# Kernel optimization log

Hardware: AMD Instinct MI355X
Metric: run time of the kernel (lower is better)

## Reference

```python
import jax, jax.numpy as jnp
import numpy as np

B, T, C = 32, 512, 1024
H, D = 16, 64
BLOCK_SIZE = 512


def setup_inputs() -> dict:
    key = jax.random.key(0)
    ks = jax.random.split(key, 6)
    s_in = 1.0 / np.sqrt(C)
    return {
        "x": jax.random.normal(ks[0], (B, T, C), dtype=jnp.float32),
        "wq": jax.random.normal(ks[1], (H, C, D), dtype=jnp.float32) * s_in,
        "wk": jax.random.normal(ks[2], (H, C, D), dtype=jnp.float32) * s_in,
        "wv": jax.random.normal(ks[3], (H, C, D), dtype=jnp.float32) * s_in,
        "w_proj": jax.random.normal(ks[4], (C, C), dtype=jnp.float32) * s_in,
        "b_proj": jax.random.normal(ks[5], (C,), dtype=jnp.float32) * 0.01,
    }


def reference(x, wq, wk, wv, w_proj, b_proj):
    b, t, c = x.shape
    # per-head projections (bias=False Linears stacked on head axis)
    q = jnp.einsum("btc,hcd->bhtd", x, wq)
    k = jnp.einsum("btc,hcd->bhtd", x, wk)
    v = jnp.einsum("btc,hcd->bhtd", x, wv)
    # NOTE: original scales by 1/sqrt(C) with C = n_embd, not head_size
    scale = 1.0 / (c ** 0.5)
    scores = jnp.einsum("bhtd,bhsd->bhts", q, k) * scale  # [B,H,T,T]
    causal = jnp.tril(jnp.ones((t, t), dtype=bool))
    scores = jnp.where(causal, scores, jnp.finfo(scores.dtype).min)
    attn = jax.nn.softmax(scores, axis=-1)
    out = jnp.einsum("bhts,bhsd->bhtd", attn, v)
    # concat heads in order -> [B,T,H*D]
    out = out.transpose(0, 2, 1, 3).reshape(b, t, -1)
    # output projection (dropout = identity in eval mode)
    return out @ w_proj + b_proj
```

## Files before the change

kernel.cpp:

```cpp
#include <hip/hip_runtime.h>

typedef unsigned int u32;
typedef unsigned short u16;
typedef __bf16 bf16x8 __attribute__((ext_vector_type(8)));
typedef float f32x4 __attribute__((ext_vector_type(4)));
typedef u16 u16x8 __attribute__((ext_vector_type(8)));
typedef u16 u16x4 __attribute__((ext_vector_type(4)));

#define DEVI static __device__ __forceinline__

DEVI u16 f2bf(float f) {
  union { float f; u32 u; } v; v.f = f;
  return (u16)((v.u + 0x7fffu + ((v.u >> 16) & 1u)) >> 16);
}

DEVI u32 cvtpk(float a, float b) {
  u32 r;
  asm("v_cvt_pk_bf16_f32 %0, %1, %2" : "=v"(r) : "v"(a), "v"(b));
  return r;
}

constexpr long QS_ = 16777216;
constexpr long XB_O    = 0;
constexpr long WQKV_O  = 16777216;
constexpr long Q_O     = 19922944;
constexpr long CTX_O   = 70254592;
constexpr long WPROJ_O = 87031808;

#define SCL_Q 0.045084220027780106f

__global__ __launch_bounds__(256) void k_prep_all(const float* __restrict__ x,
                                                  const float* __restrict__ wq,
                                                  const float* __restrict__ wk,
                                                  const float* __restrict__ wv,
                                                  const float* __restrict__ wp,
                                                  u16* __restrict__ ws) {
  __shared__ float tile[64][65];
  const int b = blockIdx.x;
  const int tid = threadIdx.x;
  if (b < 1024) {
    const float* src;
    u16* dst;
    long srs;
    if (b < 768) {
      int sel = b >> 8, rest = b & 255, h = rest >> 4, kt = rest & 15;
      const float* W = (sel == 0) ? wq : ((sel == 1) ? wk : wv);
      src = W + (long)(h * 1024 + kt * 64) * 64;
      srs = 64;
      dst = ws + WQKV_O + (long)(sel * 1024 + h * 64) * 1024 + kt * 64;
    } else {
      int b3 = b - 768, ntile = b3 >> 4, kt = b3 & 15;
      src = wp + (long)(kt * 64) * 1024 + ntile * 64;
      srs = 1024;
      dst = ws + WPROJ_O + (long)(ntile * 64) * 1024 + kt * 64;
    }
    #pragma unroll
    for (int i = 0; i < 4; ++i) {
      int idx = i * 256 + tid, r = idx >> 4, c4 = idx & 15;
      float4 v = *(const float4*)(src + (long)r * srs + c4 * 4);
      tile[r][c4 * 4 + 0] = v.x; tile[r][c4 * 4 + 1] = v.y;
      tile[r][c4 * 4 + 2] = v.z; tile[r][c4 * 4 + 3] = v.w;
    }
    __syncthreads();
    #pragma unroll
    for (int i = 0; i < 2; ++i) {
      int idx = i * 256 + tid, dr = idx >> 3, c8 = idx & 7;
      u16x8 o8;
      #pragma unroll
      for (int j = 0; j < 8; ++j) o8[j] = f2bf(tile[c8 * 8 + j][dr]);
      *(u16x8*)(dst + (long)dr * 1024 + c8 * 8) = o8;
    }
  } else {
    long id = (long)(b - 1024) * 256 + tid;
    const float4* p = (const float4*)(x + id * 8);
    float4 a = p[0], c = p[1];
    u16x8 r;
    r[0]=f2bf(a.x); r[1]=f2bf(a.y); r[2]=f2bf(a.z); r[3]=f2bf(a.w);
    r[4]=f2bf(c.x); r[5]=f2bf(c.y); r[6]=f2bf(c.z); r[7]=f2bf(c.w);
    *(u16x8*)(ws + XB_O + id * 8) = r;
  }
}

DEVI void gload16(const u16* g, u16* l) {
  __builtin_amdgcn_global_load_lds((const __attribute__((address_space(1))) u32*)g,
                                   (__attribute__((address_space(3))) u32*)l, 16, 0, 0);
}

template <int NN, int EPI, int PANELS>
__global__ __launch_bounds__(512, 2)
void k_gemm(const u16* __restrict__ A, const u16* __restrict__ Bt,
            u16* __restrict__ oq, float* __restrict__ of, const float* __restrict__ bias) {
  __shared__ u16 lds[2][4][8192];

  const int tid = threadIdx.x;
  const int lane = tid & 63;
  const int w = tid >> 6;
  const int wm = w >> 2, wn = w & 3;
  const int lg = lane >> 4, lr = lane & 15;
  const int bht = 2 + (wn >> 1);
  const int bn0 = (wn & 1) * 4;

  constexpr int NBG = NN / 256 / PANELS;
  constexpr int NG = 16 * PANELS;
  const int nwg = gridDim.x;
  const int swz = ((int)blockIdx.x & 7) * (nwg >> 3) + ((int)blockIdx.x >> 3);
  const int bm = swz / NBG, bng = swz % NBG;
  const long m0 = (long)bm * 256;

  int srcoff[2];
  #pragma unroll
  for (int r2 = 0; r2 < 2; ++r2) {
    int s = r2 * 8 + w;
    int mi = s >> 1, ks = s & 1;
    int rowl = mi * 16 + (lane >> 2);
    int colu = ks * 32 + (((lane & 3) * 8) ^ (((lane >> 5) & 1) * 16));
    srcoff[r2] = rowl * 1024 + colu;
  }
  const int fo = lr * 32 + ((lg * 8) ^ (((lr >> 3) & 1) * 16));

  const u16* At    = A  + m0 * 1024;
  const u16* Bbase = Bt + (long)bng * PANELS * 262144;

  f32x4 acc[8][4] = {};
  bf16x8 aq[2][2][2];
  bf16x8 bfr[4][2];

#define STAGE(buf_, ht_, gbase_)                                               \
  { _Pragma("unroll") for (int r_ = 0; r_ < 2; ++r_)                           \
      gload16((gbase_) + srcoff[r_], &lds[buf_][ht_][r_ * 4096 + w * 512]); }

#define LDS_AQ(set_, buf_, q_)                                                 \
  { _Pragma("unroll") for (int i_ = 0; i_ < 2; ++i_)                           \
    _Pragma("unroll") for (int ks_ = 0; ks_ < 2; ++ks_)                        \
      aq[set_][i_][ks_] = *(const bf16x8*)&lds[buf_][wm][(((q_)*2 + i_) * 2 + ks_) * 512 + fo]; }

#define LDS_BF(buf_, lo_)                                                      \
  { _Pragma("unroll") for (int j_ = 0; j_ < 2; ++j_)                           \
    _Pragma("unroll") for (int ks_ = 0; ks_ < 2; ++ks_)                        \
      bfr[(lo_) + j_][ks_] = *(const bf16x8*)&lds[buf_][bht][((bn0 + (lo_) + j_) * 2 + ks_) * 512 + fo]; }

#define QUAD8(set_, q_, lo_)                                                   \
  { __builtin_amdgcn_s_setprio(1);                                             \
    _Pragma("unroll") for (int ks_ = 0; ks_ < 2; ++ks_)                        \
    _Pragma("unroll") for (int i_ = 0; i_ < 2; ++i_)                           \
    _Pragma("unroll") for (int j_ = 0; j_ < 2; ++j_)                           \
      acc[(q_)*2 + i_][(lo_) + j_] = __builtin_amdgcn_mfma_f32_16x16x32_bf16(  \
          aq[set_][i_][ks_], bfr[(lo_) + j_][ks_], acc[(q_)*2 + i_][(lo_) + j_], 0, 0, 0); \
    __builtin_amdgcn_s_setprio(0); }

#define BARF() { asm volatile("s_barrier" ::: "memory"); }

  auto epilogue = [&](int p) {
    const int n0 = (bng * PANELS + p) * 256;
    if constexpr (EPI == 0) {
      #pragma unroll
      for (int mi = 0; mi < 8; ++mi) {
        int grow = (int)m0 + wm * 128 + mi * 16 + lg * 4;
        int b = grow >> 9, t0 = grow & 511;
        #pragma unroll
        for (int ni = 0; ni < 4; ++ni) {
          int gcol = n0 + wn * 64 + ni * 16 + lr;
          int sel = gcol >> 10, h = (gcol >> 6) & 15, d = gcol & 63;
          float scl = (sel == 0) ? SCL_Q : 1.0f;
          u16* dst = oq + (long)sel * QS_ + (((long)(b * 16 + h) * 512 + t0) * 64 + d);
          #pragma unroll
          for (int r = 0; r < 4; ++r) dst[r * 64] = f2bf(acc[mi][ni][r] * scl);
        }
      }
    } else {
      float bv[4];
      #pragma unroll
      for (int ni = 0; ni < 4; ++ni) bv[ni] = bias[n0 + wn * 64 + ni * 16 + lr];
      #pragma unroll
      for (int mi = 0; mi < 8; ++mi) {
        int grow = (int)m0 + wm * 128 + mi * 16 + lg * 4;
        #pragma unroll
        for (int ni = 0; ni < 4; ++ni) {
          int gcol = n0 + wn * 64 + ni * 16 + lr;
          #pragma unroll
          for (int r = 0; r < 4; ++r)
            of[(long)(grow + r) * NN + gcol] = acc[mi][ni][r] + bv[ni];
        }
      }
    }
  };

  STAGE(0, 0, At);
  STAGE(0, 1, At + 131072);
  STAGE(0, 2, Bbase);
  STAGE(0, 3, Bbase + 131072);
  STAGE(1, 0, At + 64);
  STAGE(1, 1, At + 131072 + 64);
  STAGE(1, 2, Bbase + 64);
  STAGE(1, 3, Bbase + 131072 + 64);
  asm volatile("s_waitcnt vmcnt(8)" ::: "memory");
  BARF();
  LDS_AQ(0, 0, 0);
  LDS_BF(0, 0);

  #pragma unroll 1
  for (int g = 0; g < NG; ++g) {
    const int buf = g & 1;
    const u16* Asrc = At + ((g + 2) & 15) * 64;
    const u16* Bsrc = Bbase + (long)((g + 2) >> 4) * 262144 + ((g + 2) & 15) * 64;

    LDS_BF(buf, 2);
    LDS_AQ(1, buf, 1);
    QUAD8(0, 0, 0);
    BARF();
    QUAD8(0, 0, 2);
    BARF();
    LDS_AQ(0, buf, 2);
    if (g + 2 < NG) { STAGE(buf, 2, Bsrc); STAGE(buf, 3, Bsrc + 131072); }
    QUAD8(1, 1, 0);
    BARF();
    QUAD8(1, 1, 2);
    BARF();
    LDS_AQ(1, buf, 3);
    QUAD8(0, 2, 0);
    BARF();
    QUAD8(0, 2, 2);
    asm volatile("s_waitcnt lgkmcnt(0)" ::: "memory");
    __builtin_amdgcn_sched_barrier(0);
    BARF();
    if (g + 2 < NG) { STAGE(buf, 0, Asrc); STAGE(buf, 1, Asrc + 131072); }
    QUAD8(1, 3, 0);
    BARF();
    if (g < NG - 2)       { asm volatile("s_waitcnt vmcnt(8)" ::: "memory"); }
    else if (g == NG - 2) { asm volatile("s_waitcnt vmcnt(0)" ::: "memory"); }
    BARF();
    if (g + 1 < NG) {
      LDS_AQ(0, buf ^ 1, 0);
      LDS_BF(buf ^ 1, 0);
    }
    QUAD8(1, 3, 2);
    BARF();

    if ((g & 15) == 15) {
      epilogue(g >> 4);
      if (g + 1 < NG) {
        #pragma unroll
        for (int mi = 0; mi < 8; ++mi)
          #pragma unroll
          for (int ni = 0; ni < 4; ++ni) acc[mi][ni] = f32x4{0.f, 0.f, 0.f, 0.f};
      }
    }
  }
#undef STAGE
#undef LDS_AQ
#undef LDS_BF
#undef QUAD8
#undef BARF
}

__global__ __launch_bounds__(256, 3)
void k_attn(const u16* __restrict__ Qp, const u16* __restrict__ Kp,
            const u16* __restrict__ Vp, u16* __restrict__ ctx) {
  __shared__ u16 k_lds[2][64 * 72];
  __shared__ u16 vt_lds[2][64 * 72];

  const int bid = blockIdx.x;
  const int qi = 3 - (bid >> 9);
  const int bh = bid & 511;
  const int tid = threadIdx.x, lane = tid & 63, w = tid >> 6;
  const int lg = lane >> 4, lr = lane & 15;
  const long base = (long)bh * (512 * 64);

  const int q0 = qi * 128 + w * 32;

#define LBAR() { asm volatile("s_waitcnt lgkmcnt(0)" ::: "memory");            \
                 __builtin_amdgcn_sched_barrier(0);                            \
                 asm volatile("s_barrier" ::: "memory"); }

  bf16x8 qf[2][2];
  #pragma unroll
  for (int mt = 0; mt < 2; ++mt)
    #pragma unroll
    for (int k2 = 0; k2 < 2; ++k2)
      qf[mt][k2] = *(const bf16x8*)(Qp + base + (long)(q0 + mt * 16 + lr) * 64 + k2 * 32 + lg * 8);

  f32x4 o[2][4] = {};
  float ls[2] = {0.f, 0.f};
  u32 pkw[2][4][2];

  const int nch = (qi + 1) * 2;
  int srow[2], scol[2], cslot[2];
  #pragma unroll
  for (int i = 0; i < 2; ++i) {
    int s = i * 256 + tid;
    srow[i] = s >> 3; scol[i] = s & 7;
    int sr = srow[i];
    cslot[i] = ((sr >> 5) << 5) + (((sr >> 2) & 3) << 3) + (((sr >> 4) & 1) << 2) + (sr & 3);
  }

  uint4 kreg[2], vreg[2];
  auto loadch = [&](int c) {
    #pragma unroll
    for (int i = 0; i < 2; ++i) {
      long go = base + (long)(c * 64 + srow[i]) * 64 + scol[i] * 8;
      kreg[i] = *(const uint4*)(Kp + go);
      vreg[i] = *(const uint4*)(Vp + go);
    }
  };
  auto writech = [&](int bsel) {
    #pragma unroll
    for (int i = 0; i < 2; ++i) {
      *(uint4*)&k_lds[bsel][srow[i] * 72 + scol[i] * 8] = kreg[i];
      union { uint4 v; u16 s[8]; } t; t.v = vreg[i];
      #pragma unroll
      for (int j = 0; j < 8; ++j)
        vt_lds[bsel][(scol[i] * 8 + j) * 72 + cslot[i]] = t.s[j];
    }
  };
  auto pv_step = [&](int vsel) {
    bf16x8 vf2[4][2];
    #pragma unroll
    for (int dt = 0; dt < 4; ++dt)
      #pragma unroll
      for (int k2 = 0; k2 < 2; ++k2)
        vf2[dt][k2] = *(const bf16x8*)&vt_lds[vsel][(dt * 16 + lr) * 72 + k2 * 32 + lg * 8];
    __builtin_amdgcn_s_setprio(1);
    #pragma unroll
    for (int k2 = 0; k2 < 2; ++k2)
      #pragma unroll
      for (int mt = 0; mt < 2; ++mt) {
        union { u32 w4[4]; bf16x8 v; } pb;
        pb.w4[0] = pkw[mt][2 * k2][0];
        pb.w4[1] = pkw[mt][2 * k2][1];
        pb.w4[2] = pkw[mt][2 * k2 + 1][0];
        pb.w4[3] = pkw[mt][2 * k2 + 1][1];
        #pragma unroll
        for (int dt = 0; dt < 4; ++dt)
          o[mt][dt] = __builtin_amdgcn_mfma_f32_16x16x32_bf16(vf2[dt][k2], pb.v, o[mt][dt], 0, 0, 0);
      }
    __builtin_amdgcn_s_setprio(0);
  };

  loadch(0);
  writech(0);
  loadch(1);
  __syncthreads();

  #pragma unroll 1
  for (int c = 0; c < nch; ++c) {
    const int bsel = c & 1;
    const bool doQK = (c * 64 <= q0 + 31);
    const bool doPV = (c >= 1) && ((c - 1) * 64 <= q0 + 31);

    bf16x8 kf2[4][2];
    if (doQK) {
      #pragma unroll
      for (int nt = 0; nt < 4; ++nt)
        #pragma unroll
        for (int k2 = 0; k2 < 2; ++k2)
          kf2[nt][k2] = *(const bf16x8*)&k_lds[bsel][(nt * 16 + lr) * 72 + k2 * 32 + lg * 8];
    }

    if (doPV) pv_step(bsel ^ 1);

    f32x4 st[2][4] = {};
    if (doQK) {
      __builtin_amdgcn_s_setprio(1);
      #pragma unroll
      for (int k2 = 0; k2 < 2; ++k2)
        #pragma unroll
        for (int mt = 0; mt < 2; ++mt)
          #pragma unroll
          for (int nt = 0; nt < 4; ++nt)
            st[mt][nt] = __builtin_amdgcn_mfma_f32_16x16x32_bf16(kf2[nt][k2], qf[mt][k2], st[mt][nt], 0, 0, 0);
      __builtin_amdgcn_s_setprio(0);

      const bool full = (c * 64 + 63 <= q0);
      #pragma unroll
      for (int mt = 0; mt < 2; ++mt) {
        const int q = q0 + mt * 16 + lr;
        if (!full) {
          #pragma unroll
          for (int nt = 0; nt < 4; ++nt)
            #pragma unroll
            for (int r = 0; r < 4; ++r) {
              int s_ = c * 64 + nt * 16 + lg * 4 + r;
              st[mt][nt][r] = (s_ <= q) ? st[mt][nt][r] : -1e30f;
            }
        }
        float ps = 0.f;
        float p[4][4];
        #pragma unroll
        for (int nt = 0; nt < 4; ++nt)
          #pragma unroll
          for (int r = 0; r < 4; ++r) {
            float pv = exp2f(st[mt][nt][r]);
            p[nt][r] = pv;
            ps += pv;
          }
        ls[mt] += ps;
        #pragma unroll
        for (int nt = 0; nt < 4; ++nt) {
          pkw[mt][nt][0] = cvtpk(p[nt][0], p[nt][1]);
          pkw[mt][nt][1] = cvtpk(p[nt][2], p[nt][3]);
        }
      }
    }

    LBAR();
    if (c + 1 < nch) writech(bsel ^ 1);
    if (c + 2 < nch) loadch(c + 2);
    LBAR();
  }

  if ((nch - 1) * 64 <= q0 + 31) pv_step((nch - 1) & 1);

  const int b = bh >> 4, h = bh & 15;
  #pragma unroll
  for (int mt = 0; mt < 2; ++mt) {
    float l = ls[mt];
    l += __shfl_xor(l, 16);
    l += __shfl_xor(l, 32);
    const float inv = 1.0f / l;
    const int t = q0 + mt * 16 + lr;
    #pragma unroll
    for (int dt = 0; dt < 4; ++dt) {
      u16x4 pk4;
      #pragma unroll
      for (int r = 0; r < 4; ++r) pk4[r] = f2bf(o[mt][dt][r] * inv);
      *(u16x4*)(ctx + ((long)(b * 512 + t)) * 1024 + h * 64 + dt * 16 + lg * 4) = pk4;
    }
  }
#undef LBAR
}

extern "C" void kernel_launch(void* const* d_in, const int* in_sizes, int n_in,
                              void* d_out, int out_size, void* d_ws, size_t ws_size,
                              hipStream_t stream) {
  const float* x  = (const float*)d_in[0];
  const float* wq = (const float*)d_in[1];
  const float* wk = (const float*)d_in[2];
  const float* wv = (const float*)d_in[3];
  const float* wp = (const float*)d_in[4];
  const float* bp = (const float*)d_in[5];
  float* out = (float*)d_out;
  u16* ws = (u16*)d_ws;

  u16* XB    = ws + XB_O;
  u16* WQKV  = ws + WQKV_O;
  u16* Qb    = ws + Q_O;
  u16* CTX   = ws + CTX_O;
  u16* WPROJ = ws + WPROJ_O;

  k_prep_all<<<9216, 256, 0, stream>>>(x, wq, wk, wv, wp, ws);
  k_gemm<3072, 0, 3><<<256, 512, 0, stream>>>(XB, WQKV, Qb, nullptr, nullptr);
  k_attn<<<2048, 256, 0, stream>>>(Qb, Qb + QS_, Qb + 2 * QS_, CTX);
  k_gemm<1024, 1, 1><<<256, 512, 0, stream>>>(CTX, WPROJ, nullptr, out, bp);
}
```

Baseline: 220.5 us.

## Double attention block to 256 query rows with 8 waves sharing K/V tiles

Measured after the change: 232.2 us. +5.3%, slower.

```diff
diff --git a/kernel.cpp b/kernel.cpp
--- a/kernel.cpp
+++ b/kernel.cpp
@@ -253,20 +253,20 @@
 #undef BARF
 }
 
-__global__ __launch_bounds__(256, 3)
+__global__ __launch_bounds__(512, 2)
 void k_attn(const u16* __restrict__ Qp, const u16* __restrict__ Kp,
             const u16* __restrict__ Vp, u16* __restrict__ ctx) {
   __shared__ u16 k_lds[2][64 * 72];
   __shared__ u16 vt_lds[2][64 * 72];
 
   const int bid = blockIdx.x;
-  const int qi = 3 - (bid >> 9);
+  const int half = 1 - (bid >> 9);
   const int bh = bid & 511;
   const int tid = threadIdx.x, lane = tid & 63, w = tid >> 6;
   const int lg = lane >> 4, lr = lane & 15;
   const long base = (long)bh * (512 * 64);
 
-  const int q0 = qi * 128 + w * 32;
+  const int q0 = half * 256 + w * 32;
 
 #define LBAR() { asm volatile("s_waitcnt lgkmcnt(0)" ::: "memory");            \
                  __builtin_amdgcn_sched_barrier(0);                            \
@@ -283,34 +283,22 @@
   float ls[2] = {0.f, 0.f};
   u32 pkw[2][4][2];
 
-  const int nch = (qi + 1) * 2;
-  int srow[2], scol[2], cslot[2];
-  #pragma unroll
-  for (int i = 0; i < 2; ++i) {
-    int s = i * 256 + tid;
-    srow[i] = s >> 3; scol[i] = s & 7;
-    int sr = srow[i];
-    cslot[i] = ((sr >> 5) << 5) + (((sr >> 2) & 3) << 3) + (((sr >> 4) & 1) << 2) + (sr & 3);
-  }
-
-  uint4 kreg[2], vreg[2];
+  const int nch = (half + 1) * 4;
+  const int srow = tid >> 3, scol = tid & 7;
+  const int cslot = ((srow >> 5) << 5) + (((srow >> 2) & 3) << 3) + (((srow >> 4) & 1) << 2) + (srow & 3);
+
+  uint4 kreg, vreg;
   auto loadch = [&](int c) {
-    #pragma unroll
-    for (int i = 0; i < 2; ++i) {
-      long go = base + (long)(c * 64 + srow[i]) * 64 + scol[i] * 8;
-      kreg[i] = *(const uint4*)(Kp + go);
-      vreg[i] = *(const uint4*)(Vp + go);
-    }
+    long go = base + (long)(c * 64 + srow) * 64 + scol * 8;
+    kreg = *(const uint4*)(Kp + go);
+    vreg = *(const uint4*)(Vp + go);
   };
   auto writech = [&](int bsel) {
-    #pragma unroll
-    for (int i = 0; i < 2; ++i) {
-      *(uint4*)&k_lds[bsel][srow[i] * 72 + scol[i] * 8] = kreg[i];
-      union { uint4 v; u16 s[8]; } t; t.v = vreg[i];
-      #pragma unroll
-      for (int j = 0; j < 8; ++j)
-        vt_lds[bsel][(scol[i] * 8 + j) * 72 + cslot[i]] = t.s[j];
-    }
+    *(uint4*)&k_lds[bsel][srow * 72 + scol * 8] = kreg;
+    union { uint4 v; u16 s[8]; } t; t.v = vreg;
+    #pragma unroll
+    for (int j = 0; j < 8; ++j)
+      vt_lds[bsel][(scol * 8 + j) * 72 + cslot] = t.s[j];
   };
   auto pv_step = [&](int vsel) {
     bf16x8 vf2[4][2];
@@ -449,6 +437,6 @@
 
   k_prep_all<<<9216, 256, 0, stream>>>(x, wq, wk, wv, wp, ws);
   k_gemm<3072, 0, 3><<<256, 512, 0, stream>>>(XB, WQKV, Qb, nullptr, nullptr);
-  k_attn<<<2048, 256, 0, stream>>>(Qb, Qb + QS_, Qb + 2 * QS_, CTX);
+  k_attn<<<1024, 512, 0, stream>>>(Qb, Qb + QS_, Qb + 2 * QS_, CTX);
   k_gemm<1024, 1, 1><<<256, 512, 0, stream>>>(CTX, WPROJ, nullptr, out, bp);
 }
```
